# Optimization experiments

Measured on AMD Instinct MI355X. Metric: run time of the kernel, lower is better.

## Reference

```python
import jax, jax.numpy as jnp
import numpy as np

B_SZ, D0, T = 64, 256, 2048   # batch, input feature dim, time dim
D1, D2 = 128, 3               # output_dim


def setup_inputs() -> dict:
    key = jax.random.key(0)
    ks = jax.random.split(key, 8)
    s = 0.02  # small init so softmax logits stay well-conditioned
    return {
        "X":       jax.random.normal(ks[0], (B_SZ, D0, T), dtype=jnp.float32),
        "W1":      jax.random.normal(ks[1], (D1, D0), dtype=jnp.float32) * s,
        "DFSMNW1": jax.random.normal(ks[2], (T, T), dtype=jnp.float32) * s,
        "DFSMNW2": jax.random.normal(ks[3], (T, T), dtype=jnp.float32) * s,
        "DFSMNW3": jax.random.normal(ks[4], (T, T), dtype=jnp.float32) * s,
        "DFSMNW4": jax.random.normal(ks[5], (T, T), dtype=jnp.float32) * s,
        "W2":      jax.random.normal(ks[6], (T, D2), dtype=jnp.float32) * s,
        "B":       jax.random.normal(ks[7], (D1, D2), dtype=jnp.float32) * s,
    }


def _dfsmn_stage(D, M_prev, W):
    # E = D @ W over time axis; legacy nn.Softmax() default for 3D input is dim=0.
    E = jnp.einsum('bot,ts->bos', D, W)
    A = jax.nn.softmax(E, axis=0)
    M = D * A + M_prev          # gated memory + running residual
    return D + M, M


def reference(X, W1, DFSMNW1, DFSMNW2, DFSMNW3, DFSMNW4, W2, B):
    # X_: [B, D1, T] = W1 @ X per sample
    X_ = jnp.einsum('od,bdt->bot', W1, X)

    # Stage 1 (no previous memory)
    A1 = jax.nn.softmax(jnp.einsum('bot,ts->bos', X_, DFSMNW1), axis=0)
    M1 = X_ * A1
    D_1 = X_ + M1

    D_2, M2 = _dfsmn_stage(D_1, M1, DFSMNW2)
    D_3, M3 = _dfsmn_stage(D_2, M2, DFSMNW3)
    D_4, _  = _dfsmn_stage(D_3, M3, DFSMNW4)

    # Output projection + bias: [B, D1, D2]
    Y = jnp.einsum('bot,td->bod', D_4, W2) + B
    return Y
```

## Files before the change

### kernel.cpp

```cpp
#include <hip/hip_runtime.h>

#define TT   2048
#define BSZ  64
#define DD0  256
#define DD1  128
#define DD2  3
#define NROW (DD1*BSZ)

typedef unsigned char u8;
typedef __attribute__((ext_vector_type(8))) short short8;
typedef __attribute__((ext_vector_type(4))) float f32x4;
typedef __attribute__((ext_vector_type(4))) unsigned short us4;
typedef __attribute__((ext_vector_type(4))) int i32x4;
typedef __attribute__((ext_vector_type(8))) int i32x8;

__device__ __forceinline__ unsigned short f2b(float f) {
  unsigned u = __builtin_bit_cast(unsigned, f);
  unsigned r = (u + 0x7fffu + ((u >> 16) & 1u)) >> 16;
  return (unsigned short)r;
}
__device__ __forceinline__ float b2f(unsigned short s) {
  unsigned u = ((unsigned)s) << 16;
  return __builtin_bit_cast(float, u);
}
__device__ __forceinline__ u8 f2f8(float x) {
  return (u8)(__builtin_amdgcn_cvt_pk_fp8_f32(x, 0.f, 0, false) & 0xff);
}
__device__ __forceinline__ unsigned f2f8x4(float a, float b, float c, float d) {
  int v = __builtin_amdgcn_cvt_pk_fp8_f32(a, b, 0, false);
  v = __builtin_amdgcn_cvt_pk_fp8_f32(c, d, v, true);
  return (unsigned)v;
}

__device__ __forceinline__ void gload16(const void* g, void* l) {
  __builtin_amdgcn_global_load_lds(
      (const __attribute__((address_space(1))) unsigned int*)(unsigned long long)g,
      (__attribute__((address_space(3))) unsigned int*)(unsigned int)(unsigned long long)l,
      16, 0, 0);
}

__global__ __launch_bounds__(256) void transpose_cvt8(
    const float* __restrict__ src, u8* __restrict__ dst)
{
  __shared__ float tile[64 * 65];
  const int c0 = blockIdx.x * 64, r0 = blockIdx.y * 64;
  const int tid = threadIdx.x;
#pragma unroll
  for (int i = 0; i < 4; ++i) {
    int e = i * 256 + tid;
    int r = e >> 4, q = e & 15;
    float4 v = *(const float4*)&src[(size_t)(r0 + r) * TT + c0 + q * 4];
    tile[r * 65 + q * 4 + 0] = v.x;
    tile[r * 65 + q * 4 + 1] = v.y;
    tile[r * 65 + q * 4 + 2] = v.z;
    tile[r * 65 + q * 4 + 3] = v.w;
  }
  __syncthreads();
#pragma unroll
  for (int i = 0; i < 4; ++i) {
    int e = i * 256 + tid;
    int c = e >> 4, q = e & 15;
    unsigned v = f2f8x4(tile[(q * 4 + 0) * 65 + c] * 8.f,
                        tile[(q * 4 + 1) * 65 + c] * 8.f,
                        tile[(q * 4 + 2) * 65 + c] * 8.f,
                        tile[(q * 4 + 3) * 65 + c] * 8.f);
    *(unsigned*)&dst[(size_t)(c0 + c) * TT + r0 + q * 4] = v;
  }
}

__global__ __launch_bounds__(256) void proj_kernel(
    const float* __restrict__ W1, const float* __restrict__ X,
    unsigned short* __restrict__ Dout, u8* __restrict__ D8)
{
  __shared__ __align__(16) unsigned short Al[128 * 256];
  const int tid = threadIdx.x;
  const int b = blockIdx.y, t0 = blockIdx.x * 128;
  const int w = tid >> 6, l = tid & 63;
  const int q4 = l >> 4;

#pragma unroll
  for (int i = 0; i < 16; ++i) {
    int id = i * 256 + tid;
    int row = id >> 5, u = id & 31;
    const float* s = &W1[row * DD0 + u * 8];
    float4 v0 = *(const float4*)s;
    float4 v1 = *(const float4*)(s + 4);
    short8 p;
    p[0] = f2b(v0.x); p[1] = f2b(v0.y); p[2] = f2b(v0.z); p[3] = f2b(v0.w);
    p[4] = f2b(v1.x); p[5] = f2b(v1.y); p[6] = f2b(v1.z); p[7] = f2b(v1.w);
    *(short8*)&Al[row * 256 + ((u ^ (row & 7)) * 8)] = p;
  }
  __syncthreads();

  f32x4 acc[8][2];
#pragma unroll
  for (int m = 0; m < 8; ++m)
#pragma unroll
    for (int n = 0; n < 2; ++n) acc[m][n] = f32x4{0.f, 0.f, 0.f, 0.f};

#pragma unroll 2
  for (int kk = 0; kk < 8; ++kk) {
    const int koff = kk * 32 + q4 * 8;
    short8 bfr[2];
#pragma unroll
    for (int n = 0; n < 2; ++n) {
      const int t = t0 + w * 32 + n * 16 + (l & 15);
      const float* xp = X + (size_t)(b * DD0 + koff) * TT + t;
      short8 p;
#pragma unroll
      for (int j = 0; j < 8; ++j) p[j] = f2b(xp[(size_t)j * TT]);
      bfr[n] = p;
    }
#pragma unroll
    for (int m = 0; m < 8; ++m) {
      int row = m * 16 + (l & 15);
      short8 a = *(const short8*)&Al[row * 256 + (((kk * 4 + q4) ^ (row & 7)) * 8)];
      acc[m][0] = __builtin_amdgcn_mfma_f32_16x16x32_bf16(a, bfr[0], acc[m][0], 0, 0, 0);
      acc[m][1] = __builtin_amdgcn_mfma_f32_16x16x32_bf16(a, bfr[1], acc[m][1], 0, 0, 0);
    }
  }
#pragma unroll
  for (int m = 0; m < 8; ++m)
#pragma unroll
    for (int n = 0; n < 2; ++n)
#pragma unroll
      for (int r = 0; r < 4; ++r) {
        int o = m * 16 + q4 * 4 + r;
        int t = t0 + w * 32 + n * 16 + (l & 15);
        size_t idx = (size_t)(o * BSZ + b) * TT + t;
        float v = acc[m][n][r];
        Dout[idx] = f2b(v);
        D8[idx] = f2f8(v * 8.f);
      }
}

__global__ __launch_bounds__(256) void init_y(
    const float* __restrict__ Bb, float* __restrict__ Y)
{
  int id = blockIdx.x * 256 + threadIdx.x;
  if (id < BSZ * DD1 * DD2) Y[id] = Bb[id % (DD1 * DD2)];
}

template <int FIRST, int LAST>
__global__ __launch_bounds__(512, 2) void stage_kernel(
    const u8* __restrict__ Din8, const unsigned short* __restrict__ DinBf,
    const u8* __restrict__ Wt8, const unsigned short* DprevBf,
    unsigned short* DoutBf, u8* __restrict__ Dout8,
    const float* __restrict__ W2, float* __restrict__ Y)
{
  __shared__ __align__(16) unsigned short lds[65536];
  char* ldsb = (char*)lds;
  const int tid = threadIdx.x, w = tid >> 6, l = tid & 63;
  const int wr = w >> 2, wc = w & 3;
  const int L = blockIdx.y * 8 + blockIdx.x;
  const int s0 = ((L >> 3) & 7) * 256;
  const int r0 = ((L & 7) * 4 + (L >> 6)) * 256;
  const u8* DinR = Din8 + (size_t)r0 * TT;
  const u8* WtR  = Wt8 + (size_t)s0 * TT;
  const int q4 = l >> 4;
  const int NT = TT / 128;

  f32x4 acc[8][4];
#pragma unroll
  for (int m = 0; m < 8; ++m)
#pragma unroll
    for (int n = 0; n < 4; ++n) acc[m][n] = f32x4{0.f, 0.f, 0.f, 0.f};

  auto STAGE = [&](int tau) {
    if (tau >= NT) return;
    const int k0 = tau * 128, buf = tau & 1;
    const int lrow = l >> 3;
    const int swz = ((l & 7) ^ lrow) << 4;
#pragma unroll
    for (int c = 0; c < 8; ++c) {
      int ch = w * 8 + c;
      const u8* base = (ch & 32) ? WtR : DinR;
      int cc = ch & 31;
      gload16(base + (size_t)(cc * 8 + lrow) * TT + k0 + swz,
              ldsb + ((ch & 32) ? 65536 : 0) + buf * 32768 + cc * 1024);
    }
  };
  auto LDA = [&](int buf, int ah, i32x8 (&ar)[4]) {
#pragma unroll
    for (int m = 0; m < 4; ++m) {
      int ra = ah * 128 + wr * 64 + m * 16 + (l & 15);
      const char* rowp = ldsb + buf * 32768 + ra * 128;
      i32x4 lo = *(const i32x4*)(rowp + (((q4 * 2 + 0) ^ (ra & 7)) * 16));
      i32x4 hi = *(const i32x4*)(rowp + (((q4 * 2 + 1) ^ (ra & 7)) * 16));
      ar[m] = __builtin_shufflevector(lo, hi, 0, 1, 2, 3, 4, 5, 6, 7);
    }
  };
  auto LDB = [&](int buf, int bh, i32x8 (&br)[2]) {
#pragma unroll
    for (int n = 0; n < 2; ++n) {
      int rb = bh * 128 + wc * 32 + n * 16 + (l & 15);
      const char* rowp = ldsb + 65536 + buf * 32768 + rb * 128;
      i32x4 lo = *(const i32x4*)(rowp + (((q4 * 2 + 0) ^ (rb & 7)) * 16));
      i32x4 hi = *(const i32x4*)(rowp + (((q4 * 2 + 1) ^ (rb & 7)) * 16));
      br[n] = __builtin_shufflevector(lo, hi, 0, 1, 2, 3, 4, 5, 6, 7);
    }
  };
  auto MM = [&](int ah, int bh, i32x8 (&ar)[4], i32x8 (&br)[2]) {
    __builtin_amdgcn_s_setprio(1);
#pragma unroll
    for (int m = 0; m < 4; ++m)
#pragma unroll
      for (int n = 0; n < 2; ++n)
        acc[ah * 4 + m][bh * 2 + n] =
            __builtin_amdgcn_mfma_scale_f32_16x16x128_f8f6f4(
                ar[m], br[n], acc[ah * 4 + m][bh * 2 + n],
                0, 0, 0, 0x7f7f7f7f, 0, 0x7f7f7f7f);
    __builtin_amdgcn_s_setprio(0);
  };

  i32x8 a[4], b0[2], b1[2];

  STAGE(0);
  asm volatile("s_waitcnt vmcnt(0)" ::: "memory");
  __builtin_amdgcn_s_barrier();

#pragma unroll 1
  for (int t = 0; t < NT; ++t) {
    const int buf = t & 1;
    STAGE(t + 1);
    LDB(buf, 0, b0);
    LDA(buf, 0, a);
    LDB(buf, 1, b1);
    MM(0, 0, a, b0);
    MM(0, 1, a, b1);
    LDA(buf, 1, a);
    MM(1, 1, a, b1);
    MM(1, 0, a, b0);
    asm volatile("s_waitcnt vmcnt(0)" ::: "memory");
    __builtin_amdgcn_s_barrier();
  }

  const int cc = l & 15;
#pragma unroll
  for (int j = 0; j < 4; ++j) {
    const int bh = j >> 1, nn = j & 1;
    const int col = bh * 128 + wc * 32 + nn * 16 + cc;
    const int u = col >> 3;
#pragma unroll
    for (int ah = 0; ah < 2; ++ah) {
      float mx = -3.0e38f;
#pragma unroll
      for (int m = 0; m < 4; ++m)
#pragma unroll
        for (int r = 0; r < 4; ++r) mx = fmaxf(mx, acc[ah * 4 + m][j][r]);
      mx = fmaxf(mx, __shfl_xor(mx, 16));
      mx = fmaxf(mx, __shfl_xor(mx, 32));
      float pr[4][4];
      float sm = 0.f;
#pragma unroll
      for (int m = 0; m < 4; ++m)
#pragma unroll
        for (int r = 0; r < 4; ++r) {
          pr[m][r] = __expf((acc[ah * 4 + m][j][r] - mx) * 0.015625f);
          sm += pr[m][r];
        }
      sm += __shfl_xor(sm, 16);
      sm += __shfl_xor(sm, 32);
      const float rs = 1.f / sm;
#pragma unroll
      for (int m = 0; m < 4; ++m)
#pragma unroll
        for (int r = 0; r < 4; ++r) {
          int row = ah * 128 + wr * 64 + m * 16 + q4 * 4 + r;
          lds[row * 256 + (((u ^ ((row >> 2) & 7)) << 3) | (col & 7))] = f2b(pr[m][r] * rs);
        }
    }
  }
  asm volatile("s_waitcnt lgkmcnt(0)" ::: "memory");
  __builtin_amdgcn_s_barrier();

#pragma unroll 2
  for (int i = 0; i < 16; ++i) {
    int unit = i * 512 + tid;
    int row = unit >> 5, u = unit & 31;
    short8 a8 = *(const short8*)&lds[row * 256 + ((u ^ ((row >> 2) & 7)) << 3)];
    size_t g = (size_t)(r0 + row) * TT + s0 + u * 8;
    short8 d8 = *(const short8*)&DinBf[g];
    short8 dp8 = {};
    if (!FIRST) dp8 = *(const short8*)&DprevBf[g];
    short8 ob;
    float dn[8];
#pragma unroll
    for (int jj = 0; jj < 8; ++jj) {
      float d = b2f((unsigned short)d8[jj]);
      float aa = b2f((unsigned short)a8[jj]);
      float mp = FIRST ? 0.f : (d - b2f((unsigned short)dp8[jj]));
      float mn = fmaf(d, aa, mp);
      dn[jj] = d + mn;
      ob[jj] = (short)f2b(dn[jj]);
    }
    if (!LAST) {
      *(short8*)&DoutBf[g] = ob;
      unsigned w0 = f2f8x4(dn[0] * 8.f, dn[1] * 8.f, dn[2] * 8.f, dn[3] * 8.f);
      unsigned w1 = f2f8x4(dn[4] * 8.f, dn[5] * 8.f, dn[6] * 8.f, dn[7] * 8.f);
      *(unsigned long long*)&Dout8[g] = (unsigned long long)w0 |
                                        ((unsigned long long)w1 << 32);
    } else {
      float p0 = 0.f, p1 = 0.f, p2 = 0.f;
#pragma unroll
      for (int jj = 0; jj < 8; ++jj) {
        const float* w2 = &W2[(size_t)(s0 + u * 8 + jj) * DD2];
        p0 = fmaf(dn[jj], w2[0], p0);
        p1 = fmaf(dn[jj], w2[1], p1);
        p2 = fmaf(dn[jj], w2[2], p2);
      }
#pragma unroll
      for (int off = 1; off < 32; off <<= 1) {
        p0 += __shfl_xor(p0, off);
        p1 += __shfl_xor(p1, off);
        p2 += __shfl_xor(p2, off);
      }
      if ((l & 31) == 0) {
        int gr = r0 + row;
        int o = gr >> 6, bb = gr & 63;
        float* y = &Y[(size_t)(bb * DD1 + o) * DD2];
        atomicAdd(&y[0], p0);
        atomicAdd(&y[1], p1);
        atomicAdd(&y[2], p2);
      }
    }
  }
}

extern "C" void kernel_launch(void* const* d_in, const int* in_sizes, int n_in,
                              void* d_out, int out_size, void* d_ws, size_t ws_size,
                              hipStream_t stream)
{
  const float* X  = (const float*)d_in[0];
  const float* W1 = (const float*)d_in[1];
  const float* DW[4] = {(const float*)d_in[2], (const float*)d_in[3],
                        (const float*)d_in[4], (const float*)d_in[5]};
  const float* W2 = (const float*)d_in[6];
  const float* Bb = (const float*)d_in[7];
  float* Y = (float*)d_out;

  u8* wsb = (u8*)d_ws;
  u8* Wt8[4];
  for (int i = 0; i < 4; ++i) Wt8[i] = wsb + (size_t)i * TT * TT;
  unsigned short* Dbf0 = (unsigned short*)(wsb + (16ull << 20));
  u8*             D80  = wsb + (48ull << 20);
  unsigned short* Dbf1 = (unsigned short*)(wsb + (64ull << 20));
  u8*             D81  = wsb + (96ull << 20);

  dim3 blk(256);
  for (int i = 0; i < 4; ++i)
    transpose_cvt8<<<dim3(TT / 64, TT / 64), blk, 0, stream>>>(DW[i], Wt8[i]);

  proj_kernel<<<dim3(TT / 128, BSZ), blk, 0, stream>>>(W1, X, Dbf0, D80);

  init_y<<<dim3((BSZ * DD1 * DD2 + 255) / 256), blk, 0, stream>>>(Bb, Y);

  dim3 sblk(512);
  dim3 sgrid(TT / 256, NROW / 256);
  stage_kernel<1, 0><<<sgrid, sblk, 0, stream>>>(D80, Dbf0, Wt8[0], Dbf0, Dbf1, D81, W2, Y);
  stage_kernel<0, 0><<<sgrid, sblk, 0, stream>>>(D81, Dbf1, Wt8[1], Dbf0, Dbf0, D80, W2, Y);
  stage_kernel<0, 0><<<sgrid, sblk, 0, stream>>>(D80, Dbf0, Wt8[2], Dbf1, Dbf1, D81, W2, Y);
  stage_kernel<0, 1><<<sgrid, sblk, 0, stream>>>(D81, Dbf1, Wt8[3], Dbf0, Dbf0, D80, W2, Y);
}
```

Baseline: 265.0 us.

## Load B operand directly from global into registers and merge weight-transpose launches

The stage GEMM no longer stages the W (B) tile through LDS. Each wave loads its B fragments directly from global memory into registers, double-buffered across iterations with a two-step unrolled loop. The MFMA order is regrouped so each A half is used against all four B fragments. The four weight transpose/convert launches are merged into one grid with a z dimension. This removes LDS traffic and LDS writes for B and saves launch overhead, but B loads are now per-wave and uncoalesced-ish (16 rows × 32 bytes), duplicated across the two wave rows, and raise register pressure.

```diff
diff --git a/kernel.cpp b/kernel.cpp
--- a/kernel.cpp
+++ b/kernel.cpp
@@ -40,9 +40,14 @@
 }
 
 __global__ __launch_bounds__(256) void transpose_cvt8(
-    const float* __restrict__ src, u8* __restrict__ dst)
+    const float* __restrict__ s0, const float* __restrict__ s1,
+    const float* __restrict__ s2, const float* __restrict__ s3,
+    u8* __restrict__ dst_all)
 {
   __shared__ float tile[64 * 65];
+  const int z = blockIdx.z;
+  const float* src = (z == 0) ? s0 : (z == 1) ? s1 : (z == 2) ? s2 : s3;
+  u8* dst = dst_all + (size_t)z * TT * TT;
   const int c0 = blockIdx.x * 64, r0 = blockIdx.y * 64;
   const int tid = threadIdx.x;
 #pragma unroll
@@ -166,18 +171,28 @@
 #pragma unroll
     for (int n = 0; n < 4; ++n) acc[m][n] = f32x4{0.f, 0.f, 0.f, 0.f};
 
-  auto STAGE = [&](int tau) {
+  auto STAGE_A = [&](int tau) {
     if (tau >= NT) return;
     const int k0 = tau * 128, buf = tau & 1;
     const int lrow = l >> 3;
     const int swz = ((l & 7) ^ lrow) << 4;
 #pragma unroll
-    for (int c = 0; c < 8; ++c) {
-      int ch = w * 8 + c;
-      const u8* base = (ch & 32) ? WtR : DinR;
-      int cc = ch & 31;
-      gload16(base + (size_t)(cc * 8 + lrow) * TT + k0 + swz,
-              ldsb + ((ch & 32) ? 65536 : 0) + buf * 32768 + cc * 1024);
+    for (int c = 0; c < 4; ++c) {
+      int ch = w * 4 + c;
+      gload16(DinR + (size_t)(ch * 8 + lrow) * TT + k0 + swz,
+              ldsb + buf * 32768 + ch * 1024);
+    }
+  };
+  auto LOADB = [&](int tau, i32x8 (&bb)[4]) {
+    if (tau >= NT) return;
+    const int k0 = tau * 128 + q4 * 32;
+#pragma unroll
+    for (int j = 0; j < 4; ++j) {
+      int rb = (j >> 1) * 128 + wc * 32 + (j & 1) * 16 + (l & 15);
+      const u8* p = WtR + (size_t)rb * TT + k0;
+      i32x4 lo = *(const i32x4*)p;
+      i32x4 hi = *(const i32x4*)(p + 16);
+      bb[j] = __builtin_shufflevector(lo, hi, 0, 1, 2, 3, 4, 5, 6, 7);
     }
   };
   auto LDA = [&](int buf, int ah, i32x8 (&ar)[4]) {
@@ -190,49 +205,39 @@
       ar[m] = __builtin_shufflevector(lo, hi, 0, 1, 2, 3, 4, 5, 6, 7);
     }
   };
-  auto LDB = [&](int buf, int bh, i32x8 (&br)[2]) {
-#pragma unroll
-    for (int n = 0; n < 2; ++n) {
-      int rb = bh * 128 + wc * 32 + n * 16 + (l & 15);
-      const char* rowp = ldsb + 65536 + buf * 32768 + rb * 128;
-      i32x4 lo = *(const i32x4*)(rowp + (((q4 * 2 + 0) ^ (rb & 7)) * 16));
-      i32x4 hi = *(const i32x4*)(rowp + (((q4 * 2 + 1) ^ (rb & 7)) * 16));
-      br[n] = __builtin_shufflevector(lo, hi, 0, 1, 2, 3, 4, 5, 6, 7);
-    }
+
+  i32x8 a[4], bA[4], bB[4];
+
+  auto BODY = [&](int t, i32x8 (&bc)[4], i32x8 (&bn)[4]) {
+    const int buf = t & 1;
+    STAGE_A(t + 1);
+    LOADB(t + 1, bn);
+#pragma unroll
+    for (int ah = 0; ah < 2; ++ah) {
+      LDA(buf, ah, a);
+      __builtin_amdgcn_s_setprio(1);
+#pragma unroll
+      for (int m = 0; m < 4; ++m)
+#pragma unroll
+        for (int j = 0; j < 4; ++j)
+          acc[ah * 4 + m][j] = __builtin_amdgcn_mfma_scale_f32_16x16x128_f8f6f4(
+              a[m], bc[j], acc[ah * 4 + m][j],
+              0, 0, 0, 0x7f7f7f7f, 0, 0x7f7f7f7f);
+      __builtin_amdgcn_s_setprio(0);
+    }
+    asm volatile("s_waitcnt vmcnt(0)" ::: "memory");
+    __builtin_amdgcn_s_barrier();
   };
-  auto MM = [&](int ah, int bh, i32x8 (&ar)[4], i32x8 (&br)[2]) {
-    __builtin_amdgcn_s_setprio(1);
-#pragma unroll
-    for (int m = 0; m < 4; ++m)
-#pragma unroll
-      for (int n = 0; n < 2; ++n)
-        acc[ah * 4 + m][bh * 2 + n] =
-            __builtin_amdgcn_mfma_scale_f32_16x16x128_f8f6f4(
-                ar[m], br[n], acc[ah * 4 + m][bh * 2 + n],
-                0, 0, 0, 0x7f7f7f7f, 0, 0x7f7f7f7f);
-    __builtin_amdgcn_s_setprio(0);
-  };
-
-  i32x8 a[4], b0[2], b1[2];
-
-  STAGE(0);
+
+  STAGE_A(0);
+  LOADB(0, bA);
   asm volatile("s_waitcnt vmcnt(0)" ::: "memory");
   __builtin_amdgcn_s_barrier();
 
 #pragma unroll 1
-  for (int t = 0; t < NT; ++t) {
-    const int buf = t & 1;
-    STAGE(t + 1);
-    LDB(buf, 0, b0);
-    LDA(buf, 0, a);
-    LDB(buf, 1, b1);
-    MM(0, 0, a, b0);
-    MM(0, 1, a, b1);
-    LDA(buf, 1, a);
-    MM(1, 1, a, b1);
-    MM(1, 0, a, b0);
-    asm volatile("s_waitcnt vmcnt(0)" ::: "memory");
-    __builtin_amdgcn_s_barrier();
+  for (int t = 0; t < NT; t += 2) {
+    BODY(t, bA, bB);
+    BODY(t + 1, bB, bA);
   }
 
   const int cc = l & 15;
@@ -340,16 +345,15 @@
   float* Y = (float*)d_out;
 
   u8* wsb = (u8*)d_ws;
-  u8* Wt8[4];
-  for (int i = 0; i < 4; ++i) Wt8[i] = wsb + (size_t)i * TT * TT;
+  u8* Wt8all = wsb;
   unsigned short* Dbf0 = (unsigned short*)(wsb + (16ull << 20));
   u8*             D80  = wsb + (48ull << 20);
   unsigned short* Dbf1 = (unsigned short*)(wsb + (64ull << 20));
   u8*             D81  = wsb + (96ull << 20);
 
   dim3 blk(256);
-  for (int i = 0; i < 4; ++i)
-    transpose_cvt8<<<dim3(TT / 64, TT / 64), blk, 0, stream>>>(DW[i], Wt8[i]);
+  transpose_cvt8<<<dim3(TT / 64, TT / 64, 4), blk, 0, stream>>>(
+      DW[0], DW[1], DW[2], DW[3], Wt8all);
 
   proj_kernel<<<dim3(TT / 128, BSZ), blk, 0, stream>>>(W1, X, Dbf0, D80);
 
@@ -357,8 +361,12 @@
 
   dim3 sblk(512);
   dim3 sgrid(TT / 256, NROW / 256);
-  stage_kernel<1, 0><<<sgrid, sblk, 0, stream>>>(D80, Dbf0, Wt8[0], Dbf0, Dbf1, D81, W2, Y);
-  stage_kernel<0, 0><<<sgrid, sblk, 0, stream>>>(D81, Dbf1, Wt8[1], Dbf0, Dbf0, D80, W2, Y);
-  stage_kernel<0, 0><<<sgrid, sblk, 0, stream>>>(D80, Dbf0, Wt8[2], Dbf1, Dbf1, D81, W2, Y);
-  stage_kernel<0, 1><<<sgrid, sblk, 0, stream>>>(D81, Dbf1, Wt8[3], Dbf0, Dbf0, D80, W2, Y);
-}
+  u8* Wt8_0 = Wt8all + 0ull * TT * TT;
+  u8* Wt8_1 = Wt8all + 1ull * TT * TT;
+  u8* Wt8_2 = Wt8all + 2ull * TT * TT;
+  u8* Wt8_3 = Wt8all + 3ull * TT * TT;
+  stage_kernel<1, 0><<<sgrid, sblk, 0, stream>>>(D80, Dbf0, Wt8_0, Dbf0, Dbf1, D81, W2, Y);
+  stage_kernel<0, 0><<<sgrid, sblk, 0, stream>>>(D81, Dbf1, Wt8_1, Dbf0, Dbf0, D80, W2, Y);
+  stage_kernel<0, 0><<<sgrid, sblk, 0, stream>>>(D80, Dbf0, Wt8_2, Dbf1, Dbf1, D81, W2, Y);
+  stage_kernel<0, 1><<<sgrid, sblk, 0, stream>>>(D81, Dbf1, Wt8_3, Dbf0, Dbf0, D80, W2, Y);
+}
```

Result: slower. 620.5 us (+134.1%).
